# Kernel optimization log

Hardware: AMD Instinct MI355X
Metric: run time of the kernel (lower is better)

The kernel has to match this reference:

```python
import jax, jax.numpy as jnp
import numpy as np

B, N, D = 4, 256, 256
NEG = -1e9


def setup_inputs() -> dict:
    key = jax.random.key(0)
    k = jax.random.split(key, 5)
    scale1 = 1.0 / np.sqrt(4 * D)
    scale2 = 1.0 / np.sqrt(D)
    return {
        "shared": jax.random.normal(k[0], (B, N, D), dtype=jnp.float32),
        "W1": jax.random.uniform(k[1], (4 * D, D), jnp.float32, -scale1, scale1),
        "b1": jax.random.uniform(k[2], (D,), jnp.float32, -scale1, scale1),
        "W2": jax.random.uniform(k[3], (D, 1), jnp.float32, -scale2, scale2),
        "b2": jax.random.uniform(k[4], (1,), jnp.float32, -scale2, scale2),
    }


def reference(shared, W1, b1, W2, b2):
    # Linear on concat([src, tgt, |src-tgt|, src*tgt]) == sum of per-block matmuls.
    Wa, Wb, Wc, Wd = W1[:D], W1[D:2 * D], W1[2 * D:3 * D], W1[3 * D:]
    src_t = jnp.einsum('bid,dh->bih', shared, Wa)        # [B,N,D]
    tgt_t = jnp.einsum('bjd,dh->bjh', shared, Wb)        # [B,N,D]
    diff = jnp.abs(shared[:, :, None, :] - shared[:, None, :, :])  # [B,N,N,D]
    prod = shared[:, :, None, :] * shared[:, None, :, :]           # [B,N,N,D]
    h = (src_t[:, :, None, :] + tgt_t[:, None, :, :]
         + jnp.einsum('bijd,dh->bijh', diff, Wc)
         + jnp.einsum('bijd,dh->bijh', prod, Wd) + b1)   # [B,N,N,D]
    h = jax.nn.silu(h)
    scores = jnp.einsum('bijh,h->bij', h, W2[:, 0]) + b2[0]  # [B,N,N]
    eye = jnp.eye(N, dtype=bool)[None]
    scores = jnp.where(eye, NEG, scores)
    return jax.nn.softmax(scores, axis=-1)
```

## Files before the change

kernel.cpp:

```cpp
#include <hip/hip_runtime.h>

#define BB 4
#define NN 256
#define DD 256
#define HH 256
#define NEGV -1.0e9f

typedef _Float16 half8 __attribute__((ext_vector_type(8)));
typedef __fp16   fp16x2 __attribute__((ext_vector_type(2)));
typedef float floatx4 __attribute__((ext_vector_type(4)));

__global__ __launch_bounds__(1024) void prep(const float* __restrict__ X,
                                             const float* __restrict__ W1,
                                             float* __restrict__ S,
                                             float* __restrict__ T,
                                             _Float16* __restrict__ Wst) {
  const int g = blockIdx.x;
  const int t = threadIdx.x;

  __shared__ float xr[4][256];
  __shared__ float part[2][4][4][256];

  if (t < 256) {
    const float wcv = W1[(size_t)(2 * DD + g) * HH + t];
    const float wdv = W1[(size_t)(3 * DD + g) * HH + t];
    const int ks = g >> 4;
    const int dd = g & 15;
    const int q  = dd >> 2;
    const int e  = (dd & 3) * 2;
    const int hgrp = t >> 4;
    const int ccw  = t & 15;
    _Float16* p = Wst + ((size_t)((ks * 16 + hgrp) * 4 + q) * 16 + ccw) * 8 + e;
    p[0] = (_Float16)wcv;
    p[1] = (_Float16)wdv;
  }

  const int row0 = g * 4;
  xr[t >> 8][t & 255] = X[(size_t)row0 * DD + t];
  __syncthreads();

  const int w    = t >> 6;
  const int lane = t & 63;
  const int r    = w >> 2;
  const int kq   = w & 3;
  const int h0   = lane * 4;
  const float* __restrict__ xrow = xr[r];
  const int dbase = kq * 64;

  float sa0 = 0.f, sa1 = 0.f, sa2 = 0.f, sa3 = 0.f;
  float sb0 = 0.f, sb1 = 0.f, sb2 = 0.f, sb3 = 0.f;
#pragma unroll 4
  for (int dd = 0; dd < 64; ++dd) {
    const int d = dbase + dd;
    const float4 wa = *(const float4*)&W1[(size_t)d * HH + h0];
    const float4 wb = *(const float4*)&W1[(size_t)(DD + d) * HH + h0];
    const float x = xrow[d];
    sa0 = fmaf(x, wa.x, sa0); sa1 = fmaf(x, wa.y, sa1);
    sa2 = fmaf(x, wa.z, sa2); sa3 = fmaf(x, wa.w, sa3);
    sb0 = fmaf(x, wb.x, sb0); sb1 = fmaf(x, wb.y, sb1);
    sb2 = fmaf(x, wb.z, sb2); sb3 = fmaf(x, wb.w, sb3);
  }
  *(float4*)&part[0][r][kq][h0] = make_float4(sa0, sa1, sa2, sa3);
  *(float4*)&part[1][r][kq][h0] = make_float4(sb0, sb1, sb2, sb3);
  __syncthreads();

  const int rr = t >> 8, hh = t & 255;
  S[(size_t)(row0 + rr) * HH + hh] =
      (part[0][rr][0][hh] + part[0][rr][1][hh]) +
      (part[0][rr][2][hh] + part[0][rr][3][hh]);
  T[(size_t)(row0 + rr) * HH + hh] =
      (part[1][rr][0][hh] + part[1][rr][1][hh]) +
      (part[1][rr][2][hh] + part[1][rr][3][hh]);
}

__device__ __forceinline__ half8 make_afrag(const float4 xi, const float4 xj) {
  fp16x2 p0 = __builtin_amdgcn_cvt_pkrtz(__builtin_fabsf(xi.x - xj.x), xi.x * xj.x);
  fp16x2 p1 = __builtin_amdgcn_cvt_pkrtz(__builtin_fabsf(xi.y - xj.y), xi.y * xj.y);
  fp16x2 p2 = __builtin_amdgcn_cvt_pkrtz(__builtin_fabsf(xi.z - xj.z), xi.z * xj.z);
  fp16x2 p3 = __builtin_amdgcn_cvt_pkrtz(__builtin_fabsf(xi.w - xj.w), xi.w * xj.w);
  uint4 u;
  u.x = __builtin_bit_cast(unsigned int, p0);
  u.y = __builtin_bit_cast(unsigned int, p1);
  u.z = __builtin_bit_cast(unsigned int, p2);
  u.w = __builtin_bit_cast(unsigned int, p3);
  return __builtin_bit_cast(half8, u);
}

#define MFMA16(af, bf, acc) acc = __builtin_amdgcn_mfma_f32_16x16x32_f16(af, bf, acc, 0, 0, 0)

__global__ __launch_bounds__(512, 4) void score_mfma(
    const float* __restrict__ X,  const float* __restrict__ b1,
    const float* __restrict__ W2, const float* __restrict__ b2,
    const float* __restrict__ S,  const float* __restrict__ T,
    const _Float16* __restrict__ Wst, float* __restrict__ Sc) {

  const int beta = blockIdx.x;
  const int b    = blockIdx.y;
  int i, qt;
  if (beta < 64)       { qt = 0; i = beta; }
  else if (beta < 192) { qt = 1; i = beta - 64; }
  else if (beta < 384) { qt = 2; i = beta - 192; }
  else                 { qt = 3; i = beta - 384; }
  const int bi    = b * NN + i;
  const int jbase = qt * 64;
  const int isUp  = qt > (i >> 6);

  const int t     = threadIdx.x;
  const int lane  = t & 63;
  const int hg    = t >> 6;
  const int q     = lane >> 4;
  const int cc    = lane & 15;

  __shared__ __align__(16) float    xi_s[DD];
  __shared__ __align__(16) _Float16 Af[32768];
  __shared__ float pre_s[HH];
  __shared__ float pre2_s[HH];
  __shared__ float w2_s[HH];
  __shared__ float sc_s[8][64];

  if (t < 256) {
    xi_s[t]  = X[(size_t)bi * DD + t];
    pre_s[t] = S[(size_t)bi * HH + t] + b1[t];
  } else {
    const int u = t - 256;
    pre2_s[u] = T[(size_t)bi * HH + u] + b1[u];
    w2_s[u]   = W2[u];
  }

  const float* __restrict__ Tb = T + (size_t)b * NN * HH;
  const float* __restrict__ Sb = S + (size_t)b * NN * HH;

  const int jloc = t & 63;
  const int jg   = jloc >> 4;
  const int ccw  = jloc & 15;
  const float* __restrict__ xjrow = X + (size_t)(b * NN + jbase + jloc) * DD;

  const char* __restrict__ bsrc = (const char*)Wst + hg * 2048 + (size_t)lane * 16;

  half8 Bf0[4], Bf1[4];
#pragma unroll
  for (int u = 0; u < 4; ++u) {
    Bf0[u] = *(const half8*)(bsrc + (size_t)u * 16384);
    Bf1[u] = *(const half8*)(bsrc + (size_t)u * 16384 + 1024);
  }

  __syncthreads();

  {
    const int sgrp = t >> 6;
#pragma unroll
    for (int idx = 0; idx < 8; ++idx) {
      const int ksqg = sgrp * 8 + idx;
      const int d0   = ksqg * 4;
      const int kg   = ksqg >> 2;
      const int qw   = ksqg & 3;
      const float4 xi4 = *(const float4*)&xi_s[d0];
      const float4 xj4 = *(const float4*)(xjrow + d0);
      *(half8*)&Af[kg * 2048 + (jg * 4 + qw) * 128 + ccw * 8] = make_afrag(xi4, xj4);
    }
  }
  __syncthreads();

  floatx4 acc0[4], acc1[4];
#pragma unroll
  for (int u = 0; u < 4; ++u) { acc0[u] = (floatx4)0.f; acc1[u] = (floatx4)0.f; }

  const _Float16* ap0 = &Af[lane * 8];
  half8 An0 = *(const half8*)(ap0);
  half8 An1 = *(const half8*)(ap0 + 512);
  half8 An2 = *(const half8*)(ap0 + 1024);
  half8 An3 = *(const half8*)(ap0 + 1536);

#pragma unroll
  for (int kg = 0; kg < 16; ++kg) {
    const int s = kg & 3;
    const half8 Bc0 = Bf0[s], Bc1 = Bf1[s];
    const half8 Ac0 = An0, Ac1 = An1, Ac2 = An2, Ac3 = An3;
    if (kg < 12) {
      const char* bk = bsrc + (size_t)(kg + 4) * 16384;
      Bf0[s] = *(const half8*)(bk);
      Bf1[s] = *(const half8*)(bk + 1024);
    }
    if (kg < 15) {
      const _Float16* ap = &Af[(kg + 1) * 2048 + lane * 8];
      An0 = *(const half8*)(ap);
      An1 = *(const half8*)(ap + 512);
      An2 = *(const half8*)(ap + 1024);
      An3 = *(const half8*)(ap + 1536);
    }
    MFMA16(Ac0, Bc0, acc0[0]); MFMA16(Ac0, Bc1, acc1[0]);
    MFMA16(Ac1, Bc0, acc0[1]); MFMA16(Ac1, Bc1, acc1[1]);
    MFMA16(Ac2, Bc0, acc0[2]); MFMA16(Ac2, Bc1, acc1[2]);
    MFMA16(Ac3, Bc0, acc0[3]); MFMA16(Ac3, Bc1, acc1[3]);
  }

  const int h0   = hg * 32 + cc;
  const int h1   = h0 + 16;
  const int jrow = jbase + q * 4;

#define EPILOGUE(VROW, PRE) {                                                   \
    float tv0[16], tv1[16];                                                     \
    _Pragma("unroll")                                                           \
    for (int u = 0; u < 16; ++u) {                                              \
      const size_t j = (size_t)(jrow + (u >> 2) * 16 + (u & 3)) * HH;           \
      tv0[u] = VROW[j + h0];                                                    \
      tv1[u] = VROW[j + h1];                                                    \
    }                                                                           \
    const float w20 = w2_s[h0], pv0 = PRE[h0];                                  \
    const float w21 = w2_s[h1], pv1 = PRE[h1];                                  \
    float p[16];                                                                \
    _Pragma("unroll")                                                           \
    for (int u = 0; u < 16; ++u) {                                              \
      const float hv0 = acc0[u >> 2][u & 3] + pv0 + tv0[u];                     \
      const float sv0 = hv0 * __builtin_amdgcn_rcpf(1.f + __expf(-hv0));        \
      p[u] = sv0 * w20;                                                         \
      const float hv1 = acc1[u >> 2][u & 3] + pv1 + tv1[u];                     \
      const float sv1 = hv1 * __builtin_amdgcn_rcpf(1.f + __expf(-hv1));        \
      p[u] = fmaf(sv1, w21, p[u]);                                              \
    }                                                                           \
    _Pragma("unroll")                                                           \
    for (int u = 0; u < 16; ++u) {                                              \
      float v = p[u];                                                           \
      v += __shfl_xor(v, 1); v += __shfl_xor(v, 2);                             \
      v += __shfl_xor(v, 4); v += __shfl_xor(v, 8);                             \
      if (cc == 0) sc_s[hg][(u >> 2) * 16 + q * 4 + (u & 3)] = v;               \
    } }

  EPILOGUE(Tb, pre_s)
  __syncthreads();

  if (t < 64) {
    float s = sc_s[0][t] + sc_s[1][t] + sc_s[2][t] + sc_s[3][t]
            + sc_s[4][t] + sc_s[5][t] + sc_s[6][t] + sc_s[7][t] + b2[0];
    const int jg2 = jbase + t;
    if (jg2 == i) s = NEGV;
    Sc[(size_t)bi * NN + jg2] = s;
  }

  if (isUp) {
    __syncthreads();
    EPILOGUE(Sb, pre2_s)
    __syncthreads();
    if (t < 64) {
      const float s = sc_s[0][t] + sc_s[1][t] + sc_s[2][t] + sc_s[3][t]
                    + sc_s[4][t] + sc_s[5][t] + sc_s[6][t] + sc_s[7][t] + b2[0];
      Sc[(size_t)(b * NN + jbase + t) * NN + i] = s;
    }
  }
#undef EPILOGUE
}

__global__ __launch_bounds__(256) void softmax_kernel(const float* __restrict__ Sc,
                                                      float* __restrict__ out) {
  const int w    = threadIdx.x >> 6;
  const int lane = threadIdx.x & 63;
  const int bi   = blockIdx.x * 4 + w;
  const float4 v = *(const float4*)&Sc[(size_t)bi * NN + lane * 4];
  float m = fmaxf(fmaxf(v.x, v.y), fmaxf(v.z, v.w));
  m = fmaxf(m, __shfl_xor(m, 1));  m = fmaxf(m, __shfl_xor(m, 2));
  m = fmaxf(m, __shfl_xor(m, 4));  m = fmaxf(m, __shfl_xor(m, 8));
  m = fmaxf(m, __shfl_xor(m, 16)); m = fmaxf(m, __shfl_xor(m, 32));
  const float e0 = __expf(v.x - m), e1 = __expf(v.y - m);
  const float e2 = __expf(v.z - m), e3 = __expf(v.w - m);
  float sum = (e0 + e1) + (e2 + e3);
  sum += __shfl_xor(sum, 1);  sum += __shfl_xor(sum, 2);
  sum += __shfl_xor(sum, 4);  sum += __shfl_xor(sum, 8);
  sum += __shfl_xor(sum, 16); sum += __shfl_xor(sum, 32);
  const float r = 1.f / sum;
  float4 o; o.x = e0 * r; o.y = e1 * r; o.z = e2 * r; o.w = e3 * r;
  *(float4*)&out[(size_t)bi * NN + lane * 4] = o;
}

extern "C" void kernel_launch(void* const* d_in, const int* in_sizes, int n_in,
                              void* d_out, int out_size, void* d_ws, size_t ws_size,
                              hipStream_t stream) {
  const float* X  = (const float*)d_in[0];
  const float* W1 = (const float*)d_in[1];
  const float* b1 = (const float*)d_in[2];
  const float* W2 = (const float*)d_in[3];
  const float* b2 = (const float*)d_in[4];
  float* out = (float*)d_out;

  float*     Sws = (float*)d_ws;
  float*     Tws = Sws + (size_t)BB * NN * HH;
  _Float16*  Wst = (_Float16*)(Tws + (size_t)BB * NN * HH);
  float*     Scw = (float*)(Wst + (size_t)16 * HH * 32);

  prep<<<256, 1024, 0, stream>>>(X, W1, Sws, Tws, Wst);
  score_mfma<<<dim3(640, BB), 512, 0, stream>>>(X, b1, W2, b2, Sws, Tws, Wst, Scw);
  softmax_kernel<<<BB * NN / 4, 256, 0, stream>>>(Scw, out);
}
```

Before: 161.6 us.

## Halve LDS A-fragment buffer and cut registers to raise score kernel occupancy

The score kernel now builds the fp16 A fragments in two halves of the K dimension, reusing an LDS buffer half the previous size, with a barrier between build and MFMA phases. The B-fragment register prefetch depth drops from four stages to two. The epilogue loads the T values for the two column groups one after the other instead of together, and launch bounds request 6 blocks per CU instead of 4. Together these lower LDS and VGPR use per block so more blocks can be resident, at the cost of extra barriers, loss of A-register prefetch and less memory-latency hiding per wave.

```diff
diff --git a/kernel.cpp b/kernel.cpp
--- a/kernel.cpp
+++ b/kernel.cpp
@@ -88,7 +88,7 @@
 
 #define MFMA16(af, bf, acc) acc = __builtin_amdgcn_mfma_f32_16x16x32_f16(af, bf, acc, 0, 0, 0)
 
-__global__ __launch_bounds__(512, 4) void score_mfma(
+__global__ __launch_bounds__(512, 6) void score_mfma(
     const float* __restrict__ X,  const float* __restrict__ b1,
     const float* __restrict__ W2, const float* __restrict__ b2,
     const float* __restrict__ S,  const float* __restrict__ T,
@@ -112,7 +112,7 @@
   const int cc    = lane & 15;
 
   __shared__ __align__(16) float    xi_s[DD];
-  __shared__ __align__(16) _Float16 Af[32768];
+  __shared__ __align__(16) _Float16 Af[16384];
   __shared__ float pre_s[HH];
   __shared__ float pre2_s[HH];
   __shared__ float w2_s[HH];
@@ -137,61 +137,53 @@
 
   const char* __restrict__ bsrc = (const char*)Wst + hg * 2048 + (size_t)lane * 16;
 
-  half8 Bf0[4], Bf1[4];
-#pragma unroll
-  for (int u = 0; u < 4; ++u) {
+  floatx4 acc0[4], acc1[4];
+#pragma unroll
+  for (int u = 0; u < 4; ++u) { acc0[u] = (floatx4)0.f; acc1[u] = (floatx4)0.f; }
+
+  half8 Bf0[2], Bf1[2];
+#pragma unroll
+  for (int u = 0; u < 2; ++u) {
     Bf0[u] = *(const half8*)(bsrc + (size_t)u * 16384);
     Bf1[u] = *(const half8*)(bsrc + (size_t)u * 16384 + 1024);
   }
 
-  __syncthreads();
-
-  {
-    const int sgrp = t >> 6;
-#pragma unroll
-    for (int idx = 0; idx < 8; ++idx) {
-      const int ksqg = sgrp * 8 + idx;
-      const int d0   = ksqg * 4;
-      const int kg   = ksqg >> 2;
-      const int qw   = ksqg & 3;
+#pragma unroll 1
+  for (int half = 0; half < 2; ++half) {
+    __syncthreads();
+
+#pragma unroll
+    for (int idx = 0; idx < 4; ++idx) {
+      const int ksq = hg * 4 + idx;
+      const int d0  = (half * 32 + ksq) * 4;
+      const int ksl = ksq >> 2;
+      const int qw  = ksq & 3;
       const float4 xi4 = *(const float4*)&xi_s[d0];
       const float4 xj4 = *(const float4*)(xjrow + d0);
-      *(half8*)&Af[kg * 2048 + (jg * 4 + qw) * 128 + ccw * 8] = make_afrag(xi4, xj4);
+      *(half8*)&Af[(ksl * 16 + jg * 4 + qw) * 128 + ccw * 8] = make_afrag(xi4, xj4);
     }
-  }
-  __syncthreads();
-
-  floatx4 acc0[4], acc1[4];
-#pragma unroll
-  for (int u = 0; u < 4; ++u) { acc0[u] = (floatx4)0.f; acc1[u] = (floatx4)0.f; }
-
-  const _Float16* ap0 = &Af[lane * 8];
-  half8 An0 = *(const half8*)(ap0);
-  half8 An1 = *(const half8*)(ap0 + 512);
-  half8 An2 = *(const half8*)(ap0 + 1024);
-  half8 An3 = *(const half8*)(ap0 + 1536);
-
-#pragma unroll
-  for (int kg = 0; kg < 16; ++kg) {
-    const int s = kg & 3;
-    const half8 Bc0 = Bf0[s], Bc1 = Bf1[s];
-    const half8 Ac0 = An0, Ac1 = An1, Ac2 = An2, Ac3 = An3;
-    if (kg < 12) {
-      const char* bk = bsrc + (size_t)(kg + 4) * 16384;
-      Bf0[s] = *(const half8*)(bk);
-      Bf1[s] = *(const half8*)(bk + 1024);
+    __syncthreads();
+
+#pragma unroll
+    for (int ksl = 0; ksl < 8; ++ksl) {
+      const int s = ksl & 1;
+      const half8 Bc0 = Bf0[s], Bc1 = Bf1[s];
+      {
+        const int kn = (half * 8 + ksl + 2) & 15;
+        const char* bk = bsrc + (size_t)kn * 16384;
+        Bf0[s] = *(const half8*)(bk);
+        Bf1[s] = *(const half8*)(bk + 1024);
+      }
+      const _Float16* ap = &Af[ksl * 2048 + lane * 8];
+      const half8 A0 = *(const half8*)(ap);
+      const half8 A1 = *(const half8*)(ap + 512);
+      const half8 A2 = *(const half8*)(ap + 1024);
+      const half8 A3 = *(const half8*)(ap + 1536);
+      MFMA16(A0, Bc0, acc0[0]); MFMA16(A0, Bc1, acc1[0]);
+      MFMA16(A1, Bc0, acc0[1]); MFMA16(A1, Bc1, acc1[1]);
+      MFMA16(A2, Bc0, acc0[2]); MFMA16(A2, Bc1, acc1[2]);
+      MFMA16(A3, Bc0, acc0[3]); MFMA16(A3, Bc1, acc1[3]);
     }
-    if (kg < 15) {
-      const _Float16* ap = &Af[(kg + 1) * 2048 + lane * 8];
-      An0 = *(const half8*)(ap);
-      An1 = *(const half8*)(ap + 512);
-      An2 = *(const half8*)(ap + 1024);
-      An3 = *(const half8*)(ap + 1536);
-    }
-    MFMA16(Ac0, Bc0, acc0[0]); MFMA16(Ac0, Bc1, acc1[0]);
-    MFMA16(Ac1, Bc0, acc0[1]); MFMA16(Ac1, Bc1, acc1[1]);
-    MFMA16(Ac2, Bc0, acc0[2]); MFMA16(Ac2, Bc1, acc1[2]);
-    MFMA16(Ac3, Bc0, acc0[3]); MFMA16(Ac3, Bc1, acc1[3]);
   }
 
   const int h0   = hg * 32 + cc;
@@ -199,24 +191,36 @@
   const int jrow = jbase + q * 4;
 
 #define EPILOGUE(VROW, PRE) {                                                   \
-    float tv0[16], tv1[16];                                                     \
-    _Pragma("unroll")                                                           \
-    for (int u = 0; u < 16; ++u) {                                              \
-      const size_t j = (size_t)(jrow + (u >> 2) * 16 + (u & 3)) * HH;           \
-      tv0[u] = VROW[j + h0];                                                    \
-      tv1[u] = VROW[j + h1];                                                    \
-    }                                                                           \
     const float w20 = w2_s[h0], pv0 = PRE[h0];                                  \
     const float w21 = w2_s[h1], pv1 = PRE[h1];                                  \
     float p[16];                                                                \
-    _Pragma("unroll")                                                           \
-    for (int u = 0; u < 16; ++u) {                                              \
-      const float hv0 = acc0[u >> 2][u & 3] + pv0 + tv0[u];                     \
-      const float sv0 = hv0 * __builtin_amdgcn_rcpf(1.f + __expf(-hv0));        \
-      p[u] = sv0 * w20;                                                         \
-      const float hv1 = acc1[u >> 2][u & 3] + pv1 + tv1[u];                     \
-      const float sv1 = hv1 * __builtin_amdgcn_rcpf(1.f + __expf(-hv1));        \
-      p[u] = fmaf(sv1, w21, p[u]);                                              \
+    {                                                                           \
+      float tv[16];                                                             \
+      _Pragma("unroll")                                                         \
+      for (int u = 0; u < 16; ++u) {                                            \
+        const size_t j = (size_t)(jrow + (u >> 2) * 16 + (u & 3)) * HH;         \
+        tv[u] = VROW[j + h0];                                                   \
+      }                                                                         \
+      _Pragma("unroll")                                                         \
+      for (int u = 0; u < 16; ++u) {                                            \
+        const float hv0 = acc0[u >> 2][u & 3] + pv0 + tv[u];                    \
+        const float sv0 = hv0 * __builtin_amdgcn_rcpf(1.f + __expf(-hv0));      \
+        p[u] = sv0 * w20;                                                       \
+      }                                                                         \
+    }                                                                           \
+    {                                                                           \
+      float tv[16];                                                             \
+      _Pragma("unroll")                                                         \
+      for (int u = 0; u < 16; ++u) {                                            \
+        const size_t j = (size_t)(jrow + (u >> 2) * 16 + (u & 3)) * HH;         \
+        tv[u] = VROW[j + h1];                                                   \
+      }                                                                         \
+      _Pragma("unroll")                                                         \
+      for (int u = 0; u < 16; ++u) {                                            \
+        const float hv1 = acc1[u >> 2][u & 3] + pv1 + tv[u];                    \
+        const float sv1 = hv1 * __builtin_amdgcn_rcpf(1.f + __expf(-hv1));      \
+        p[u] = fmaf(sv1, w21, p[u]);                                            \
+      }                                                                         \
     }                                                                           \
     _Pragma("unroll")                                                           \
     for (int u = 0; u < 16; ++u) {                                              \
```

Measured after the change: 275.5 us. 70.5% more time.
